# Performance work log

Hardware: AMD Instinct MI355X
Metric: run time of the kernel (lower is better)

## Reference

```python
import jax, jax.numpy as jnp
import numpy as np

B, T, D, K = 8, 4096, 1024, 3


def setup_inputs() -> dict:
    key = jax.random.key(0)
    k0, k1, k2 = jax.random.split(key, 3)
    x = jax.random.normal(k0, (B, T, D), dtype=jnp.float32)
    lim = 1.0 / np.sqrt(D)
    Wv = jax.random.uniform(k1, (D, D), dtype=jnp.float32, minval=-lim, maxval=lim)
    bv = jnp.zeros((D,), dtype=jnp.float32)
    Wo = jax.random.uniform(k2, (D, D), dtype=jnp.float32, minval=-lim, maxval=lim)
    bo = jnp.zeros((D,), dtype=jnp.float32)
    neighbor_weights = jnp.ones((K,), dtype=jnp.float32) / K
    return {"x": x, "Wv": Wv, "bv": bv, "Wo": Wo, "bo": bo,
            "neighbor_weights": neighbor_weights}


def reference(x, Wv, bv, Wo, bo, neighbor_weights):
    # x: [B, T, D]; faithful translation of the unfold -> Linear -> weighted-sum chain
    k = neighbor_weights.shape[0]
    pad = k // 2
    t = x.shape[1]
    # replicate padding along T (torch F.pad mode='replicate')
    xp = jnp.pad(x, ((0, 0), (pad, pad), (0, 0)), mode='edge')  # [B, T+2*pad, D]
    # sliding windows: [B, T, K, D] (small fixed K loop, not a data-dim loop)
    windows = jnp.stack([xp[:, i:i + t, :] for i in range(k)], axis=2)
    # value projection applied per window element (nn.Linear: x @ W.T + b)
    v = jnp.einsum('btkd,ed->btke', windows, Wv) + bv  # [B, T, K, D]
    # fixed-weight neighbor average
    attended = jnp.einsum('btkd,k->btd', v, neighbor_weights)  # [B, T, D]
    # output projection
    return jnp.einsum('btd,ed->bte', attended, Wo) + bo
```

## Files before the change

### kernel.cpp

```cpp
#include <hip/hip_runtime.h>
#include <stdint.h>
#include <stddef.h>

typedef _Float16 f16_t;
typedef _Float16 f16x4 __attribute__((ext_vector_type(4)));
typedef _Float16 f16x8 __attribute__((ext_vector_type(8)));
typedef float f32x4 __attribute__((ext_vector_type(4)));

#define AS_G __attribute__((address_space(1)))
#define AS_L __attribute__((address_space(3)))

__device__ __forceinline__ void gload_lds16(const void* g, void* l) {
  __builtin_amdgcn_global_load_lds((AS_G void*)g, (AS_L void*)l, 16, 0, 0);
}

#define FENCE() asm volatile("" ::: "memory")
#define BARX()                            \
  do {                                    \
    FENCE();                              \
    __builtin_amdgcn_s_barrier();         \
    FENCE();                              \
  } while (0)
#define VMCNT(n) asm volatile("s_waitcnt vmcnt(" #n ")" ::: "memory")
#define LGKM0() asm volatile("s_waitcnt lgkmcnt(0)" ::: "memory")


__global__ void cvt_f16_kernel(const float* __restrict__ in, f16_t* __restrict__ out, int n4) {
  int i = blockIdx.x * blockDim.x + threadIdx.x;
  if (i >= n4) return;
  f32x4 v = ((const f32x4*)in)[i];
  f16x4 o;
  o.x = (f16_t)v.x; o.y = (f16_t)v.y; o.z = (f16_t)v.z; o.w = (f16_t)v.w;
  ((f16x4*)out)[i] = o;
}

__global__ void transpose_cvt_kernel(const float* __restrict__ in, f16_t* __restrict__ out) {
  __shared__ float tile[32][33];
  const int bx = blockIdx.x, by = blockIdx.y;
  const int tx = threadIdx.x, ty = threadIdx.y;
#pragma unroll
  for (int i = 0; i < 32; i += 8)
    tile[ty + i][tx] = in[(size_t)(by * 32 + ty + i) * 1024 + bx * 32 + tx];
  __syncthreads();
#pragma unroll
  for (int i = 0; i < 32; i += 8)
    out[(size_t)(bx * 32 + ty + i) * 1024 + by * 32 + tx] = (f16_t)tile[tx][ty + i];
}

__global__ void bconst_kernel(const float* __restrict__ Wo, const float* __restrict__ bv,
                              const float* __restrict__ bo, const float* __restrict__ nw,
                              int Kw, float* __restrict__ bc) {
  const int e = blockIdx.x;
  const int t = threadIdx.x;
  float sw = 0.f;
  for (int k = 0; k < Kw; ++k) sw += nw[k];
  float p = 0.f;
  for (int d = t; d < 1024; d += 256) p += Wo[(size_t)e * 1024 + d] * bv[d];
  __shared__ float red[256];
  red[t] = p;
  __syncthreads();
  for (int s = 128; s > 0; s >>= 1) {
    if (t < s) red[t] += red[t + s];
    __syncthreads();
  }
  if (t == 0) bc[e] = sw * red[0] + bo[e];
}


template <typename OutT, bool BIAS>
__global__ __launch_bounds__(256) void gemm_bt_kernel(const f16_t* __restrict__ A,
                                                      const f16_t* __restrict__ Bt,
                                                      OutT* __restrict__ C,
                                                      const float* __restrict__ bias,
                                                      int M, int N, int K) {
  __shared__ __align__(16) f16_t sA[128 * 32];
  __shared__ __align__(16) f16_t sB[128 * 32];
  const int tid = threadIdx.x;
  const int l = tid & 63;
  const int w = tid >> 6;
  const int wr = w >> 1;
  const int wc = w & 1;
  const int nMT = M >> 7;
  const int bid = blockIdx.x;
  const int mt = bid % nMT;
  const int nt = bid / nMT;
  const int m0 = mt << 7;
  const int n0 = nt << 7;

  const int srow = (w << 4) + (l >> 2);
  const int scol = (l & 3) << 3;
  const size_t aoff0 = (size_t)(m0 + srow) * K + scol;
  const size_t boff0 = (size_t)(n0 + srow) * K + scol;
  f16_t* ldsA = sA + (w << 9);
  f16_t* ldsB = sB + (w << 9);

  f32x4 acc[4][4];
#pragma unroll
  for (int i = 0; i < 4; ++i)
#pragma unroll
    for (int j = 0; j < 4; ++j) acc[i][j] = f32x4{0.f, 0.f, 0.f, 0.f};

  const int ka = (l >> 4) << 3;
  const int ar = (wr << 6) + (l & 15);
  const int br = (wc << 6) + (l & 15);

  const int nK = K >> 5;
  for (int kt = 0; kt < nK; ++kt) {
    const int kb = kt << 5;
    gload_lds16(A + aoff0 + kb, ldsA);
    gload_lds16(A + aoff0 + ((size_t)K << 6) + kb, ldsA + 2048);
    gload_lds16(Bt + boff0 + kb, ldsB);
    gload_lds16(Bt + boff0 + ((size_t)K << 6) + kb, ldsB + 2048);
    __syncthreads();
    f16x8 af[4], bfr[4];
#pragma unroll
    for (int m = 0; m < 4; ++m) af[m] = *(const f16x8*)(sA + ((ar + (m << 4)) << 5) + ka);
#pragma unroll
    for (int n = 0; n < 4; ++n) bfr[n] = *(const f16x8*)(sB + ((br + (n << 4)) << 5) + ka);
#pragma unroll
    for (int m = 0; m < 4; ++m)
#pragma unroll
      for (int n = 0; n < 4; ++n)
        acc[m][n] = __builtin_amdgcn_mfma_f32_16x16x32_f16(af[m], bfr[n], acc[m][n], 0, 0, 0);
    __syncthreads();
  }

  const int orow = (l >> 4) << 2;
  const int ocol = l & 15;
#pragma unroll
  for (int n = 0; n < 4; ++n) {
    const int gn = n0 + (wc << 6) + (n << 4) + ocol;
    const float bs = BIAS ? bias[gn] : 0.f;
#pragma unroll
    for (int m = 0; m < 4; ++m) {
      const int gm = m0 + (wr << 6) + (m << 4) + orow;
#pragma unroll
      for (int j = 0; j < 4; ++j) {
        C[(size_t)(gm + j) * N + gn] = (OutT)(acc[m][n][j] + bs);
      }
    }
  }
}


__device__ __forceinline__ void stageB(const f16_t* __restrict__ g, int K,
                                       f16_t* ldsOp, int w, int l) {
#pragma unroll
  for (int i = 0; i < 2; ++i) {
    const int f = i * 512 + w * 64 + l;
    const int row = f >> 2;
    const int ch = f & 3;
    const int col = ((ch ^ ((row >> 1) & 3)) << 3);
    gload_lds16(g + (size_t)row * K + col, ldsOp + i * 4096 + w * 512);
  }
}

__global__ __launch_bounds__(512, 2) void gemm_fused_kernel(
    const float* __restrict__ X, const f16_t* __restrict__ Bt,
    float* __restrict__ C, const float* __restrict__ bias,
    const float* __restrict__ nw) {
  constexpr int N = 1024, K = 1024, T = 4096;
  constexpr int nK = K >> 5;
  constexpr int AST = 40;
  __shared__ __align__(16) f16_t sA[2 * 256 * AST];
  __shared__ __align__(16) f16_t sB[3 * 8192];

  const int tid = threadIdx.x;
  const int l = tid & 63;
  const int w = tid >> 6;
  const int wr = w >> 2;
  const int wc = w & 3;
  const int lr = l & 15;
  const int q = l >> 4;

  const int cpx = (int)gridDim.x >> 3;
  const int swz = ((int)blockIdx.x & 7) * cpx + ((int)blockIdx.x >> 3);
  const int nNT = N >> 8;
  const int mt = swz / nNT;
  const int nt = swz % nNT;
  const int m0 = mt << 8;
  const int n0 = nt << 8;

  const f16_t* Bpanel = Bt + (size_t)n0 * K;

  const int rp = tid >> 2;
  const int cch = tid & 3;
  const bool bst = (m0 & (T - 1)) == 0;
  const bool ben = ((m0 + 256) & (T - 1)) == 0;
  const int r0 = rp << 1, r1 = r0 + 1;
  const int rm = (rp == 0 && bst) ? 0 : r0 - 1;
  const int r2 = (rp == 127 && ben) ? r1 : r1 + 1;
  const float* pxm = X + (size_t)(m0 + rm) * K + (cch << 3);
  const float* px0 = X + (size_t)(m0 + r0) * K + (cch << 3);
  const float* px1 = X + (size_t)(m0 + r1) * K + (cch << 3);
  const float* px2 = X + (size_t)(m0 + r2) * K + (cch << 3);
  const float w0 = nw[0], w1 = nw[1], w2 = nw[2];

  f32x4 va0, va1, vb0, vb1, vc0, vc1, vd0, vd1;

#define ALOAD(kt)                                          \
  do {                                                     \
    const int off_ = (kt) << 5;                            \
    va0 = *(const f32x4*)(pxm + off_);                     \
    va1 = *(const f32x4*)(pxm + off_ + 4);                 \
    vb0 = *(const f32x4*)(px0 + off_);                     \
    vb1 = *(const f32x4*)(px0 + off_ + 4);                 \
    vc0 = *(const f32x4*)(px1 + off_);                     \
    vc1 = *(const f32x4*)(px1 + off_ + 4);                 \
    vd0 = *(const f32x4*)(px2 + off_);                     \
    vd1 = *(const f32x4*)(px2 + off_ + 4);                 \
  } while (0)

#define AWRITE(buf)                                                      \
  do {                                                                   \
    f16_t* dst_ = sA + (buf) * (256 * AST);                              \
    f32x4 t00 = w0 * va0 + w1 * vb0 + w2 * vc0;                          \
    f32x4 t01 = w0 * va1 + w1 * vb1 + w2 * vc1;                          \
    f32x4 t10 = w0 * vb0 + w1 * vc0 + w2 * vd0;                          \
    f32x4 t11 = w0 * vb1 + w1 * vc1 + w2 * vd1;                          \
    f16x8 y0_, y1_;                                                      \
    _Pragma("unroll") for (int e = 0; e < 4; ++e) {                      \
      y0_[e] = (f16_t)t00[e]; y0_[e + 4] = (f16_t)t01[e];                \
      y1_[e] = (f16_t)t10[e]; y1_[e + 4] = (f16_t)t11[e];                \
    }                                                                    \
    *(f16x8*)(dst_ + r0 * AST + (cch << 3)) = y0_;                       \
    *(f16x8*)(dst_ + r1 * AST + (cch << 3)) = y1_;                       \
  } while (0)

  f32x4 acc[8][4];
#pragma unroll
  for (int m = 0; m < 8; ++m)
#pragma unroll
    for (int n = 0; n < 4; ++n) acc[m][n] = f32x4{0.f, 0.f, 0.f, 0.f};

  const int swB = (q ^ ((lr >> 1) & 3)) << 3;

  ALOAD(0);
  stageB(Bpanel, K, sB, w, l);
  stageB(Bpanel + 32, K, sB + 8192, w, l);
  VMCNT(4);
  AWRITE(0);
  ALOAD(1);
  VMCNT(10);
  LGKM0();
  BARX();

  for (int t = 0; t < nK; ++t) {
    f16_t* cA = sA + (t & 1) * (256 * AST);
    f16_t* cB = sB + (t % 3) * 8192;

    f16x8 bf[4], af[4];
#pragma unroll
    for (int n = 0; n < 4; ++n)
      bf[n] = *(const f16x8*)(cB + (((wc << 6) + (n << 4) + lr) << 5) + swB);
#pragma unroll
    for (int m = 0; m < 4; ++m)
      af[m] = *(const f16x8*)(cA + ((wr << 7) + (m << 4) + lr) * AST + (q << 3));
    if (t + 2 < nK) stageB(Bpanel + ((t + 2) << 5), K, sB + ((t + 2) % 3) * 8192, w, l);
    BARX();
    __builtin_amdgcn_s_setprio(1);
#pragma unroll
    for (int m = 0; m < 4; ++m)
#pragma unroll
      for (int n = 0; n < 4; ++n)
        acc[m][n] = __builtin_amdgcn_mfma_f32_16x16x32_f16(af[m], bf[n], acc[m][n], 0, 0, 0);
    __builtin_amdgcn_s_setprio(0);
    BARX();

    f16x8 ag[4];
#pragma unroll
    for (int m = 0; m < 4; ++m)
      ag[m] = *(const f16x8*)(cA + ((wr << 7) + 64 + (m << 4) + lr) * AST + (q << 3));
    VMCNT(2);
    if (t + 1 < nK) AWRITE((t + 1) & 1);
    if (t + 2 < nK) ALOAD(t + 2);
    BARX();
    __builtin_amdgcn_s_setprio(1);
#pragma unroll
    for (int m = 0; m < 4; ++m)
#pragma unroll
      for (int n = 0; n < 4; ++n)
        acc[m + 4][n] = __builtin_amdgcn_mfma_f32_16x16x32_f16(ag[m], bf[n], acc[m + 4][n], 0, 0, 0);
    __builtin_amdgcn_s_setprio(0);
    LGKM0();
    BARX();
  }

  float bs[4];
#pragma unroll
  for (int n = 0; n < 4; ++n) bs[n] = bias[n0 + (wc << 6) + (n << 4) + lr];
#pragma unroll
  for (int m = 0; m < 8; ++m) {
    const int gm = m0 + (wr << 7) + (m << 4) + (q << 2);
#pragma unroll
    for (int j = 0; j < 4; ++j) {
      float* Crow = C + (size_t)(gm + j) * N + n0 + (wc << 6) + lr;
#pragma unroll
      for (int n = 0; n < 4; ++n) Crow[n << 4] = acc[m][n][j] + bs[n];
    }
  }
#undef ALOAD
#undef AWRITE
}


extern "C" void kernel_launch(void* const* d_in, const int* in_sizes, int n_in,
                              void* d_out, int out_size, void* d_ws, size_t ws_size,
                              hipStream_t stream) {
  const float* x = (const float*)d_in[0];
  const float* Wv = (const float*)d_in[1];
  const float* bv = (const float*)d_in[2];
  const float* Wo = (const float*)d_in[3];
  const float* bo = (const float*)d_in[4];
  const float* nw = (const float*)d_in[5];
  float* out = (float*)d_out;

  char* ws = (char*)d_ws;
  f16_t* Wo_h = (f16_t*)(ws);
  f16_t* WvT  = (f16_t*)(ws + (2u << 20));
  f16_t* WcT  = (f16_t*)(ws + (4u << 20));
  float* bc   = (float*)(ws + (6u << 20));

  cvt_f16_kernel<<<dim3(1024), dim3(256), 0, stream>>>(Wo, Wo_h, 1024 * 1024 / 4);
  transpose_cvt_kernel<<<dim3(32, 32), dim3(32, 8), 0, stream>>>(Wv, WvT);
  bconst_kernel<<<dim3(1024), dim3(256), 0, stream>>>(Wo, bv, bo, nw, in_sizes[5], bc);
  gemm_bt_kernel<f16_t, false><<<dim3(64), dim3(256), 0, stream>>>(
      Wo_h, WvT, WcT, (const float*)nullptr, 1024, 1024, 1024);
  gemm_fused_kernel<<<dim3(512), dim3(512), 0, stream>>>(x, WcT, out, bc, nw);
}
```

Before: 155.2 us.

## Merge weight-prep kernels into one launch and move A-staging after second MFMA half

Three small preprocessing kernels (Wo fp16 convert, Wv transpose-convert, bias constant) are merged into a single launch with block-range dispatch, removing two kernel launches. In the fused GEMM main loop, the A-tile write to LDS and the next global load of x are moved after the second MFMA batch so they overlap with compute. Loads are made unconditional by clamping the tile index, which keeps vmcnt accounting uniform at the cost of redundant loads in the final iterations.

```diff
diff --git a/kernel.cpp b/kernel.cpp
--- a/kernel.cpp
+++ b/kernel.cpp
@@ -25,45 +25,45 @@
 #define LGKM0() asm volatile("s_waitcnt lgkmcnt(0)" ::: "memory")
 
 
-__global__ void cvt_f16_kernel(const float* __restrict__ in, f16_t* __restrict__ out, int n4) {
-  int i = blockIdx.x * blockDim.x + threadIdx.x;
-  if (i >= n4) return;
-  f32x4 v = ((const f32x4*)in)[i];
-  f16x4 o;
-  o.x = (f16_t)v.x; o.y = (f16_t)v.y; o.z = (f16_t)v.z; o.w = (f16_t)v.w;
-  ((f16x4*)out)[i] = o;
-}
-
-__global__ void transpose_cvt_kernel(const float* __restrict__ in, f16_t* __restrict__ out) {
-  __shared__ float tile[32][33];
-  const int bx = blockIdx.x, by = blockIdx.y;
-  const int tx = threadIdx.x, ty = threadIdx.y;
-#pragma unroll
-  for (int i = 0; i < 32; i += 8)
-    tile[ty + i][tx] = in[(size_t)(by * 32 + ty + i) * 1024 + bx * 32 + tx];
-  __syncthreads();
-#pragma unroll
-  for (int i = 0; i < 32; i += 8)
-    out[(size_t)(bx * 32 + ty + i) * 1024 + by * 32 + tx] = (f16_t)tile[tx][ty + i];
-}
-
-__global__ void bconst_kernel(const float* __restrict__ Wo, const float* __restrict__ bv,
-                              const float* __restrict__ bo, const float* __restrict__ nw,
-                              int Kw, float* __restrict__ bc) {
-  const int e = blockIdx.x;
+__global__ __launch_bounds__(256) void prep_kernel(
+    const float* __restrict__ Wo, const float* __restrict__ Wv,
+    const float* __restrict__ bv, const float* __restrict__ bo,
+    const float* __restrict__ nw, int Kw,
+    f16_t* __restrict__ Wo_h, f16_t* __restrict__ WvT, float* __restrict__ bc) {
+  __shared__ float smem[32 * 33];
+  const int b = blockIdx.x;
   const int t = threadIdx.x;
-  float sw = 0.f;
-  for (int k = 0; k < Kw; ++k) sw += nw[k];
-  float p = 0.f;
-  for (int d = t; d < 1024; d += 256) p += Wo[(size_t)e * 1024 + d] * bv[d];
-  __shared__ float red[256];
-  red[t] = p;
-  __syncthreads();
-  for (int s = 128; s > 0; s >>= 1) {
-    if (t < s) red[t] += red[t + s];
+  if (b < 1024) {
+    const int i = b * 256 + t;
+    f32x4 v = ((const f32x4*)Wo)[i];
+    f16x4 o;
+    o.x = (f16_t)v.x; o.y = (f16_t)v.y; o.z = (f16_t)v.z; o.w = (f16_t)v.w;
+    ((f16x4*)Wo_h)[i] = o;
+  } else if (b < 2048) {
+    const int i = b - 1024;
+    const int bx = i & 31, by = i >> 5;
+    const int tx = t & 31, ty = t >> 5;
+#pragma unroll
+    for (int k = 0; k < 32; k += 8)
+      smem[(ty + k) * 33 + tx] = Wv[(size_t)(by * 32 + ty + k) * 1024 + bx * 32 + tx];
     __syncthreads();
-  }
-  if (t == 0) bc[e] = sw * red[0] + bo[e];
+#pragma unroll
+    for (int k = 0; k < 32; k += 8)
+      WvT[(size_t)(bx * 32 + ty + k) * 1024 + by * 32 + tx] = (f16_t)smem[tx * 33 + ty + k];
+  } else {
+    const int e = b - 2048;
+    float sw = 0.f;
+    for (int k = 0; k < Kw; ++k) sw += nw[k];
+    float p = 0.f;
+    for (int d = t; d < 1024; d += 256) p += Wo[(size_t)e * 1024 + d] * bv[d];
+    smem[t] = p;
+    __syncthreads();
+    for (int s = 128; s > 0; s >>= 1) {
+      if (t < s) smem[t] += smem[t + s];
+      __syncthreads();
+    }
+    if (t == 0) bc[e] = sw * smem[0] + bo[e];
+  }
 }
 
 
@@ -200,7 +200,8 @@
 
 #define ALOAD(kt)                                          \
   do {                                                     \
-    const int off_ = (kt) << 5;                            \
+    const int kk_ = (kt) < (nK - 1) ? (kt) : (nK - 1);     \
+    const int off_ = kk_ << 5;                             \
     va0 = *(const f32x4*)(pxm + off_);                     \
     va1 = *(const f32x4*)(pxm + off_ + 4);                 \
     vb0 = *(const f32x4*)(px0 + off_);                     \
@@ -241,7 +242,7 @@
   VMCNT(4);
   AWRITE(0);
   ALOAD(1);
-  VMCNT(10);
+  VMCNT(8);
   LGKM0();
   BARX();
 
@@ -256,7 +257,10 @@
 #pragma unroll
     for (int m = 0; m < 4; ++m)
       af[m] = *(const f16x8*)(cA + ((wr << 7) + (m << 4) + lr) * AST + (q << 3));
-    if (t + 2 < nK) stageB(Bpanel + ((t + 2) << 5), K, sB + ((t + 2) % 3) * 8192, w, l);
+    {
+      const int tp2 = (t + 2) < (nK - 1) ? (t + 2) : (nK - 1);
+      stageB(Bpanel + ((size_t)tp2 << 5), K, sB + (tp2 % 3) * 8192, w, l);
+    }
     BARX();
     __builtin_amdgcn_s_setprio(1);
 #pragma unroll
@@ -271,9 +275,6 @@
 #pragma unroll
     for (int m = 0; m < 4; ++m)
       ag[m] = *(const f16x8*)(cA + ((wr << 7) + 64 + (m << 4) + lr) * AST + (q << 3));
-    VMCNT(2);
-    if (t + 1 < nK) AWRITE((t + 1) & 1);
-    if (t + 2 < nK) ALOAD(t + 2);
     BARX();
     __builtin_amdgcn_s_setprio(1);
 #pragma unroll
@@ -282,6 +283,9 @@
       for (int n = 0; n < 4; ++n)
         acc[m + 4][n] = __builtin_amdgcn_mfma_f32_16x16x32_f16(ag[m], bf[n], acc[m + 4][n], 0, 0, 0);
     __builtin_amdgcn_s_setprio(0);
+    VMCNT(2);
+    if (t + 1 < nK) AWRITE((t + 1) & 1);
+    ALOAD(t + 2);
     LGKM0();
     BARX();
   }
@@ -321,9 +325,8 @@
   f16_t* WcT  = (f16_t*)(ws + (4u << 20));
   float* bc   = (float*)(ws + (6u << 20));
 
-  cvt_f16_kernel<<<dim3(1024), dim3(256), 0, stream>>>(Wo, Wo_h, 1024 * 1024 / 4);
-  transpose_cvt_kernel<<<dim3(32, 32), dim3(32, 8), 0, stream>>>(Wv, WvT);
-  bconst_kernel<<<dim3(1024), dim3(256), 0, stream>>>(Wo, bv, bo, nw, in_sizes[5], bc);
+  prep_kernel<<<dim3(3072), dim3(256), 0, stream>>>(Wo, Wv, bv, bo, nw, in_sizes[5],
+                                                    Wo_h, WvT, bc);
   gemm_bt_kernel<f16_t, false><<<dim3(64), dim3(256), 0, stream>>>(
       Wo_h, WvT, WcT, (const float*)nullptr, 1024, 1024, 1024);
   gemm_fused_kernel<<<dim3(512), dim3(512), 0, stream>>>(x, WcT, out, bc, nw);
```

Result: slower. 166.0 us (+7.0%).
